# Kernel tuning notes

Hardware: AMD Instinct MI355X
Metric: run time of the kernel (lower is better)

Reference implementation:

```python
import jax, jax.numpy as jnp
import numpy as np
import math

NHEAD = 16
FACTOR = 5


def setup_inputs() -> dict:
    key = jax.random.key(0)
    ks = jax.random.split(key, 10)
    B, L, Dm = 2, 2048, 1024
    x = jax.random.normal(ks[0], (B, L, Dm), dtype=jnp.float32)
    w = lambda k: jax.random.normal(k, (Dm, Dm), dtype=jnp.float32) * 0.02
    b = lambda k: jax.random.normal(k, (Dm,), dtype=jnp.float32) * 0.02
    return {
        "x": x,
        "Wq": w(ks[1]), "bq": b(ks[2]),
        "Wk": w(ks[3]), "bk": b(ks[4]),
        "Wv": w(ks[5]), "bv": b(ks[6]),
        "Wo": w(ks[7]), "bo": b(ks[8]),
    }


def reference(x, Wq, bq, Wk, bk, Wv, bv, Wo, bo):
    B, L, Dm = x.shape
    H = NHEAD
    D = Dm // H
    # U = number of top scores kept per query row (ProbSparse sparsity level)
    U = min(L, int(FACTOR * math.log(L)) if L > 1 else L)

    def proj(W, b):
        # torch Linear: x @ W^T + b ; then [B,L,H,D] -> [B,H,L,D]
        return (x @ W.T + b).reshape(B, L, H, D).transpose(0, 2, 1, 3)

    Q = proj(Wq, bq)
    K = proj(Wk, bk)
    V = proj(Wv, bv)

    scores = jnp.einsum("bhqd,bhkd->bhqk", Q, K) / math.sqrt(D)  # [B,H,L,L]
    # kth-largest score per row; keep entries >= threshold (ties kept, matching torch semantics)
    thresh = jax.lax.top_k(scores, U)[0][..., -1:]  # [B,H,L,1]
    scores = jnp.where(scores < thresh, -jnp.inf, scores)
    attn = jax.nn.softmax(scores, axis=-1)  # dropout is identity in eval
    context = jnp.einsum("bhqk,bhkd->bhqd", attn, V)
    context = context.transpose(0, 2, 1, 3).reshape(B, L, Dm)
    return context @ Wo.T + bo
```

## Files before the change

### kernel.cpp

```cpp
#include <hip/hip_runtime.h>
#include <math.h>

#define BB 2
#define LL 2048
#define DM 1024
#define NH 16
#define HD 64

__device__ __forceinline__ unsigned mono32(float f) {
    unsigned u = __float_as_uint(f);
    return (u & 0x80000000u) ? ~u : (u | 0x80000000u);
}
__device__ __forceinline__ float unmono32(unsigned m) {
    const unsigned u = (m & 0x80000000u) ? (m & 0x7FFFFFFFu) : ~m;
    return __uint_as_float(u);
}

__global__ __launch_bounds__(256) void transpose1024(
    const float* __restrict__ in, float* __restrict__ out)
{
    __shared__ float t[32][33];
    const int bx = blockIdx.x * 32, by = blockIdx.y * 32;
    const int tx = threadIdx.x & 31, ty = threadIdx.x >> 5;
    for (int r = ty; r < 32; r += 8)
        t[r][tx] = in[(size_t)(by + r) * DM + bx + tx];
    __syncthreads();
    for (int r = ty; r < 32; r += 8)
        out[(size_t)(bx + r) * DM + by + tx] = t[tx][r];
}

__global__ __launch_bounds__(256) void proj_emul(
    const float* __restrict__ x, const float* __restrict__ Wt,
    const float* __restrict__ bias, float* __restrict__ outp)
{
    __shared__ float xs[8][DM];
    const int tid = threadIdx.x;
    const int n   = blockIdx.x * 256 + tid;
    const int m0  = blockIdx.y * 8;

    for (int i = tid; i < 8 * 256; i += 256) {
        const int r = i >> 8, c4 = (i & 255) << 2;
        *(float4*)&xs[r][c4] = *(const float4*)&x[(size_t)(m0 + r) * DM + c4];
    }
    __syncthreads();

    const int kbound[4] = {0, 384, 704, 1024};

    float S[8] = {0, 0, 0, 0, 0, 0, 0, 0};
#pragma unroll
    for (int p = 0; p < 3; p++) {
        float P[8] = {0, 0, 0, 0, 0, 0, 0, 0};
        for (int k = kbound[p]; k < kbound[p + 1]; k++) {
            const float w = Wt[(size_t)k * DM + n];
#pragma unroll
            for (int m = 0; m < 8; m++) P[m] = fmaf(xs[m][k], w, P[m]);
        }
#pragma unroll
        for (int m = 0; m < 8; m++) S[m] += P[m];
    }

    const int h = n / HD, d = n % HD;
#pragma unroll
    for (int m = 0; m < 8; m++) {
        const int mm = m0 + m;
        const int b = mm / LL, l = mm % LL;
        outp[(((size_t)b * NH + h) * LL + l) * HD + d] = S[m] + bias[n];
    }
}

template <int MODE>
__global__ __launch_bounds__(256) void gemm_f32(
    const float* __restrict__ A, const float* __restrict__ W,
    const float* __restrict__ bias, float* __restrict__ out,
    int M, int N, int K)
{
    __shared__ float As[16][64];
    __shared__ float Bs[16][64];
    const int tid = threadIdx.x;
    const int m0 = blockIdx.y * 64;
    const int n0 = blockIdx.x * 64;
    const int tx = tid & 15, ty = tid >> 4;
    const int lr = tid >> 2, lc = (tid & 3) * 4;

    float acc[4][4] = {};

    for (int k0 = 0; k0 < K; k0 += 16) {
        float4 a4 = *(const float4*)&A[(size_t)(m0 + lr) * K + k0 + lc];
        float4 b4 = *(const float4*)&W[(size_t)(n0 + lr) * K + k0 + lc];
        __syncthreads();
        As[lc + 0][lr] = a4.x; As[lc + 1][lr] = a4.y;
        As[lc + 2][lr] = a4.z; As[lc + 3][lr] = a4.w;
        Bs[lc + 0][lr] = b4.x; Bs[lc + 1][lr] = b4.y;
        Bs[lc + 2][lr] = b4.z; Bs[lc + 3][lr] = b4.w;
        __syncthreads();
#pragma unroll
        for (int kk = 0; kk < 16; kk++) {
            float4 av = *(const float4*)&As[kk][ty * 4];
            float4 bv = *(const float4*)&Bs[kk][tx * 4];
            float a[4] = {av.x, av.y, av.z, av.w};
            float b[4] = {bv.x, bv.y, bv.z, bv.w};
#pragma unroll
            for (int i = 0; i < 4; i++)
#pragma unroll
                for (int j = 0; j < 4; j++)
                    acc[i][j] = fmaf(a[i], b[j], acc[i][j]);
        }
    }

#pragma unroll
    for (int i = 0; i < 4; i++) {
        const int m = m0 + ty * 4 + i;
#pragma unroll
        for (int j = 0; j < 4; j++) {
            const int n = n0 + tx * 4 + j;
            const float v = acc[i][j] + bias[n];
            if (MODE == 0) {
                const int b = m / LL, l = m % LL;
                const int h = n / HD, d = n % HD;
                out[(((size_t)b * NH + h) * LL + l) * HD + d] = v;
            } else {
                out[(size_t)m * N + n] = v;
            }
        }
    }
}

__global__ __launch_bounds__(256) void score_np(
    const float* __restrict__ Qf, const float* __restrict__ Kf,
    unsigned* __restrict__ scw, int bh0)
{
#pragma clang fp contract(off)
    const int tid  = threadIdx.x;
    const int lane = tid & 63;
    const int wv   = tid >> 6;
    const int l0   = blockIdx.x * 8;
    const int bhl  = blockIdx.y;
    const int bh   = bh0 + bhl;

    __shared__ float kt[2][64][68];
    __shared__ float qsh[8][64];

    const float* __restrict__ Kb = Kf + (size_t)bh * LL * HD;

    if (tid < 128) {
        const int r = tid >> 4, d4 = tid & 15;
        *(float4*)&qsh[r][d4 * 4] =
            *(const float4*)&Qf[((size_t)bh * LL + l0 + r) * HD + d4 * 4];
    }
#pragma unroll
    for (int i = 0; i < 4; i++) {
        const int idx = i * 256 + tid;
        *(float4*)&kt[0][idx >> 4][(idx & 15) * 4] =
            *(const float4*)&Kb[(size_t)(idx >> 4) * HD + (idx & 15) * 4];
    }
    __syncthreads();

    const int r0 = wv * 2, r1 = r0 + 1;
    unsigned* __restrict__ s0 = scw + ((size_t)bhl * LL + l0 + r0) * LL;
    unsigned* __restrict__ s1 = scw + ((size_t)bhl * LL + l0 + r1) * LL;

    for (int tile = 0; tile < 32; tile++) {
        const int buf = tile & 1;
        float4 pf0, pf1, pf2, pf3;
        if (tile < 31) {
            const float* src = Kb + (size_t)(tile + 1) * 64 * HD;
            pf0 = *(const float4*)&src[(size_t)((0 * 256 + tid) >> 4) * HD + ((0 * 256 + tid) & 15) * 4];
            pf1 = *(const float4*)&src[(size_t)((1 * 256 + tid) >> 4) * HD + ((1 * 256 + tid) & 15) * 4];
            pf2 = *(const float4*)&src[(size_t)((2 * 256 + tid) >> 4) * HD + ((2 * 256 + tid) & 15) * 4];
            pf3 = *(const float4*)&src[(size_t)((3 * 256 + tid) >> 4) * HD + ((3 * 256 + tid) & 15) * 4];
        }

        float axA = 0, ayA = 0, azA = 0, awA = 0;
        float axB = 0, ayB = 0, azB = 0, awB = 0;
        const float* krow = &kt[buf][lane][0];
        const float* qA = &qsh[r0][0];
        const float* qB = &qsh[r1][0];
#pragma unroll
        for (int t = 0; t < 4; t++) {
#pragma unroll
            for (int sub = 3; sub >= 0; sub--) {
                const int d4 = 4 * t + sub;
                const float4 kf = *(const float4*)&krow[d4 * 4];
                const float4 qa = *(const float4*)&qA[d4 * 4];
                const float4 qb = *(const float4*)&qB[d4 * 4];
                axA = qa.x * kf.x + axA; ayA = qa.y * kf.y + ayA;
                azA = qa.z * kf.z + azA; awA = qa.w * kf.w + awA;
                axB = qb.x * kf.x + axB; ayB = qb.y * kf.y + ayB;
                azB = qb.z * kf.z + azB; awB = qb.w * kf.w + awB;
            }
        }
        s0[tile * 64 + lane] = mono32(((axA + ayA) + (azA + awA)) * 0.125f);
        s1[tile * 64 + lane] = mono32(((axB + ayB) + (azB + awB)) * 0.125f);

        if (tile < 31) {
            *(float4*)&kt[buf ^ 1][(0 * 256 + tid) >> 4][((0 * 256 + tid) & 15) * 4] = pf0;
            *(float4*)&kt[buf ^ 1][(1 * 256 + tid) >> 4][((1 * 256 + tid) & 15) * 4] = pf1;
            *(float4*)&kt[buf ^ 1][(2 * 256 + tid) >> 4][((2 * 256 + tid) & 15) * 4] = pf2;
            *(float4*)&kt[buf ^ 1][(3 * 256 + tid) >> 4][((3 * 256 + tid) & 15) * 4] = pf3;
            __syncthreads();
        }
    }
}

__global__ __launch_bounds__(256) void select_np(
    const unsigned* __restrict__ scw, const float* __restrict__ Vf,
    float* __restrict__ ctx, int U, int bh0)
{
#pragma clang fp contract(off)
    const int tid  = threadIdx.x;
    const int lane = tid & 63;
    const int wv   = tid >> 6;
    const int l0   = blockIdx.x * 8;
    const int bhl  = blockIdx.y;
    const int bh   = bh0 + bhl;
    const int b    = bh / NH;
    const int h    = bh % NH;

    __shared__ float wls[8][64];
    __shared__ int   kls[8][64];

    const unsigned long long laneLT = (1ull << lane) - 1ull;
    const float* __restrict__ Vb = Vf + (size_t)bh * LL * HD;

#pragma unroll
    for (int rr8 = 0; rr8 < 2; rr8++) {
        const int rr = wv * 2 + rr8;
        const unsigned* __restrict__ srow =
            scw + ((size_t)bhl * LL + l0 + rr) * LL;

        unsigned mv[32];
#pragma unroll
        for (int j = 0; j < 32; j++) mv[j] = srow[lane + 64 * j];

        unsigned lo = 0u, hi = 0xFFFFFFFFu;
        while (lo < hi) {
            const unsigned span = hi - lo;
            const unsigned mid = lo + (span >> 1) + (span & 1u);
            int c = 0;
#pragma unroll
            for (int j = 0; j < 32; j++)
                c += (int)__popcll(__ballot(mv[j] >= mid));
            if (c >= U) lo = mid; else hi = mid - 1u;
        }

        unsigned mk = 0;
#pragma unroll
        for (int j = 0; j < 32; j++)
            if (mv[j] >= lo) mk = (mv[j] > mk) ? mv[j] : mk;
#pragma unroll
        for (int off = 32; off > 0; off >>= 1) {
            const unsigned o = __shfl_xor(mk, off, 64);
            mk = (o > mk) ? o : mk;
        }
        const float mx = unmono32(mk);

        int n = 0;
#pragma unroll
        for (int j = 0; j < 32; j++) {
            const bool p = (mv[j] >= lo);
            const unsigned long long ball = __ballot(p);
            if (p) {
                const int pos = n + (int)__popcll(ball & laneLT);
                if (pos < 64) {
                    kls[rr][pos] = lane + 64 * j;
                    wls[rr][pos] = expf(unmono32(mv[j]) - mx);
                }
            }
            n += (int)__popcll(ball);
        }
        if (n > 64) n = 64;

        float dl = (lane < n) ? wls[rr][lane] : 0.0f;
#pragma unroll
        for (int off = 32; off > 0; off >>= 1) dl += __shfl_xor(dl, off, 64);
        const float rden = 1.0f / dl;

        float acc = 0.0f;
        for (int c = 0; c < n; c++)
            acc = fmaf(wls[rr][c], Vb[(size_t)kls[rr][c] * HD + lane], acc);

        ctx[((size_t)b * LL + l0 + rr) * DM + h * HD + lane] = acc * rden;
    }
}

extern "C" void kernel_launch(void* const* d_in, const int* in_sizes, int n_in,
                              void* d_out, int out_size, void* d_ws, size_t ws_size,
                              hipStream_t stream)
{
    const float* x  = (const float*)d_in[0];
    const float* Wq = (const float*)d_in[1];
    const float* bq = (const float*)d_in[2];
    const float* Wk = (const float*)d_in[3];
    const float* bk = (const float*)d_in[4];
    const float* Wv = (const float*)d_in[5];
    const float* bv = (const float*)d_in[6];
    const float* Wo = (const float*)d_in[7];
    const float* bo = (const float*)d_in[8];
    float* out = (float*)d_out;

    const size_t E = (size_t)BB * NH * LL * HD;
    float* Wt1 = (float*)d_ws;
    float* Wt2 = Wt1 + (size_t)DM * DM;
    float* Qf  = Wt2 + (size_t)DM * DM;
    float* Kf  = Qf + E;
    float* Vf  = Kf + E;
    float* ctx = Vf + E;
    unsigned* scw = (unsigned*)(ctx + E);

    int U = (int)(5.0 * log((double)LL));
    if (U > LL) U = LL;

    const size_t base_bytes = (size_t)72 * 1024 * 1024;
    const size_t per_bh = (size_t)LL * LL * 4;
    size_t avail = (ws_size > base_bytes) ? (ws_size - base_bytes) : 0;
    int chunk = (int)(avail / per_bh);
    if (chunk < 1) chunk = 1;
    if (chunk > 8) chunk = 8;

    const int M = BB * LL;
    dim3 blk(256);
    dim3 gT(DM / 32, DM / 32);
    dim3 gP(DM / 256, M / 8);
    dim3 g64(DM / 64, M / 64);

    hipLaunchKernelGGL(transpose1024, gT, blk, 0, stream, Wq, Wt1);
    hipLaunchKernelGGL(transpose1024, gT, blk, 0, stream, Wk, Wt2);
    hipLaunchKernelGGL(proj_emul, gP, blk, 0, stream, x, Wt1, bq, Qf);
    hipLaunchKernelGGL(proj_emul, gP, blk, 0, stream, x, Wt2, bk, Kf);
    hipLaunchKernelGGL((gemm_f32<0>), g64, blk, 0, stream, x, Wv, bv, Vf, M, DM, DM);

    for (int bh0 = 0; bh0 < BB * NH; bh0 += chunk) {
        int nb = BB * NH - bh0;
        if (nb > chunk) nb = chunk;
        dim3 gA(LL / 8, nb);
        hipLaunchKernelGGL(score_np,  gA, blk, 0, stream, Qf, Kf, scw, bh0);
        hipLaunchKernelGGL(select_np, gA, blk, 0, stream, scw, Vf, ctx, U, bh0);
    }

    hipLaunchKernelGGL((gemm_f32<1>), g64, blk, 0, stream, ctx, Wo, bo, out, M, DM, DM);
}
```

Measured before the change: 1.948 ms.

## Increase per-thread tiling in projection and score kernels for more data reuse

The projection kernel now has each block cover all output columns for 8 rows, with each thread computing 4 columns via float4 weight loads and vectorised shared x reads. This removes redundant x staging and cuts per-FMA load overhead. The score kernel processes 16 query rows per block (4 per wave), so each K tile loaded into shared memory is reused twice as much. The cost is higher register pressure and fewer blocks in both kernels.

```diff
diff --git a/kernel.cpp b/kernel.cpp
--- a/kernel.cpp
+++ b/kernel.cpp
@@ -35,8 +35,8 @@
 {
     __shared__ float xs[8][DM];
     const int tid = threadIdx.x;
-    const int n   = blockIdx.x * 256 + tid;
-    const int m0  = blockIdx.y * 8;
+    const int n4  = tid * 4;
+    const int m0  = blockIdx.x * 8;
 
     for (int i = tid; i < 8 * 256; i += 256) {
         const int r = i >> 8, c4 = (i & 255) << 2;
@@ -45,26 +45,53 @@
     __syncthreads();
 
     const int kbound[4] = {0, 384, 704, 1024};
-
-    float S[8] = {0, 0, 0, 0, 0, 0, 0, 0};
+    float S[8][4] = {};
 #pragma unroll
     for (int p = 0; p < 3; p++) {
-        float P[8] = {0, 0, 0, 0, 0, 0, 0, 0};
-        for (int k = kbound[p]; k < kbound[p + 1]; k++) {
-            const float w = Wt[(size_t)k * DM + n];
-#pragma unroll
-            for (int m = 0; m < 8; m++) P[m] = fmaf(xs[m][k], w, P[m]);
-        }
-#pragma unroll
-        for (int m = 0; m < 8; m++) S[m] += P[m];
-    }
-
-    const int h = n / HD, d = n % HD;
+        float P[8][4] = {};
+        for (int k = kbound[p]; k < kbound[p + 1]; k += 4) {
+            const float4 w0 = *(const float4*)&Wt[(size_t)(k + 0) * DM + n4];
+            const float4 w1 = *(const float4*)&Wt[(size_t)(k + 1) * DM + n4];
+            const float4 w2 = *(const float4*)&Wt[(size_t)(k + 2) * DM + n4];
+            const float4 w3 = *(const float4*)&Wt[(size_t)(k + 3) * DM + n4];
+#pragma unroll
+            for (int m = 0; m < 8; m++) {
+                const float4 xv = *(const float4*)&xs[m][k];
+                P[m][0] = fmaf(xv.x, w0.x, P[m][0]);
+                P[m][1] = fmaf(xv.x, w0.y, P[m][1]);
+                P[m][2] = fmaf(xv.x, w0.z, P[m][2]);
+                P[m][3] = fmaf(xv.x, w0.w, P[m][3]);
+                P[m][0] = fmaf(xv.y, w1.x, P[m][0]);
+                P[m][1] = fmaf(xv.y, w1.y, P[m][1]);
+                P[m][2] = fmaf(xv.y, w1.z, P[m][2]);
+                P[m][3] = fmaf(xv.y, w1.w, P[m][3]);
+                P[m][0] = fmaf(xv.z, w2.x, P[m][0]);
+                P[m][1] = fmaf(xv.z, w2.y, P[m][1]);
+                P[m][2] = fmaf(xv.z, w2.z, P[m][2]);
+                P[m][3] = fmaf(xv.z, w2.w, P[m][3]);
+                P[m][0] = fmaf(xv.w, w3.x, P[m][0]);
+                P[m][1] = fmaf(xv.w, w3.y, P[m][1]);
+                P[m][2] = fmaf(xv.w, w3.z, P[m][2]);
+                P[m][3] = fmaf(xv.w, w3.w, P[m][3]);
+            }
+        }
+#pragma unroll
+        for (int m = 0; m < 8; m++) {
+#pragma unroll
+            for (int j = 0; j < 4; j++) S[m][j] += P[m][j];
+        }
+    }
+
+    const float4 b4v = *(const float4*)&bias[n4];
+    const int h = n4 / HD, d0 = n4 % HD;
 #pragma unroll
     for (int m = 0; m < 8; m++) {
         const int mm = m0 + m;
         const int b = mm / LL, l = mm % LL;
-        outp[(((size_t)b * NH + h) * LL + l) * HD + d] = S[m] + bias[n];
+        float4 o;
+        o.x = S[m][0] + b4v.x; o.y = S[m][1] + b4v.y;
+        o.z = S[m][2] + b4v.z; o.w = S[m][3] + b4v.w;
+        *(float4*)&outp[(((size_t)b * NH + h) * LL + l) * HD + d0] = o;
     }
 }
 
@@ -133,19 +160,19 @@
     const int tid  = threadIdx.x;
     const int lane = tid & 63;
     const int wv   = tid >> 6;
-    const int l0   = blockIdx.x * 8;
+    const int l0   = blockIdx.x * 16;
     const int bhl  = blockIdx.y;
     const int bh   = bh0 + bhl;
 
     __shared__ float kt[2][64][68];
-    __shared__ float qsh[8][64];
+    __shared__ float qsh[16][64];
 
     const float* __restrict__ Kb = Kf + (size_t)bh * LL * HD;
 
-    if (tid < 128) {
-        const int r = tid >> 4, d4 = tid & 15;
-        *(float4*)&qsh[r][d4 * 4] =
-            *(const float4*)&Qf[((size_t)bh * LL + l0 + r) * HD + d4 * 4];
+    {
+        const int r = tid >> 4, d4q = tid & 15;
+        *(float4*)&qsh[r][d4q * 4] =
+            *(const float4*)&Qf[((size_t)bh * LL + l0 + r) * HD + d4q * 4];
     }
 #pragma unroll
     for (int i = 0; i < 4; i++) {
@@ -155,9 +182,11 @@
     }
     __syncthreads();
 
-    const int r0 = wv * 2, r1 = r0 + 1;
-    unsigned* __restrict__ s0 = scw + ((size_t)bhl * LL + l0 + r0) * LL;
-    unsigned* __restrict__ s1 = scw + ((size_t)bhl * LL + l0 + r1) * LL;
+    const int r0 = wv * 4;
+    unsigned* __restrict__ s0 = scw + ((size_t)bhl * LL + l0 + r0 + 0) * LL;
+    unsigned* __restrict__ s1 = scw + ((size_t)bhl * LL + l0 + r0 + 1) * LL;
+    unsigned* __restrict__ s2 = scw + ((size_t)bhl * LL + l0 + r0 + 2) * LL;
+    unsigned* __restrict__ s3 = scw + ((size_t)bhl * LL + l0 + r0 + 3) * LL;
 
     for (int tile = 0; tile < 32; tile++) {
         const int buf = tile & 1;
@@ -170,27 +199,39 @@
             pf3 = *(const float4*)&src[(size_t)((3 * 256 + tid) >> 4) * HD + ((3 * 256 + tid) & 15) * 4];
         }
 
-        float axA = 0, ayA = 0, azA = 0, awA = 0;
-        float axB = 0, ayB = 0, azB = 0, awB = 0;
+        float ax0 = 0, ay0 = 0, az0 = 0, aw0 = 0;
+        float ax1 = 0, ay1 = 0, az1 = 0, aw1 = 0;
+        float ax2 = 0, ay2 = 0, az2 = 0, aw2 = 0;
+        float ax3 = 0, ay3 = 0, az3 = 0, aw3 = 0;
         const float* krow = &kt[buf][lane][0];
-        const float* qA = &qsh[r0][0];
-        const float* qB = &qsh[r1][0];
+        const float* q0 = &qsh[r0 + 0][0];
+        const float* q1 = &qsh[r0 + 1][0];
+        const float* q2 = &qsh[r0 + 2][0];
+        const float* q3 = &qsh[r0 + 3][0];
 #pragma unroll
         for (int t = 0; t < 4; t++) {
 #pragma unroll
             for (int sub = 3; sub >= 0; sub--) {
                 const int d4 = 4 * t + sub;
                 const float4 kf = *(const float4*)&krow[d4 * 4];
-                const float4 qa = *(const float4*)&qA[d4 * 4];
-                const float4 qb = *(const float4*)&qB[d4 * 4];
-                axA = qa.x * kf.x + axA; ayA = qa.y * kf.y + ayA;
-                azA = qa.z * kf.z + azA; awA = qa.w * kf.w + awA;
-                axB = qb.x * kf.x + axB; ayB = qb.y * kf.y + ayB;
-                azB = qb.z * kf.z + azB; awB = qb.w * kf.w + awB;
+                const float4 qa = *(const float4*)&q0[d4 * 4];
+                const float4 qb = *(const float4*)&q1[d4 * 4];
+                const float4 qc = *(const float4*)&q2[d4 * 4];
+                const float4 qd = *(const float4*)&q3[d4 * 4];
+                ax0 = qa.x * kf.x + ax0; ay0 = qa.y * kf.y + ay0;
+                az0 = qa.z * kf.z + az0; aw0 = qa.w * kf.w + aw0;
+                ax1 = qb.x * kf.x + ax1; ay1 = qb.y * kf.y + ay1;
+                az1 = qb.z * kf.z + az1; aw1 = qb.w * kf.w + aw1;
+                ax2 = qc.x * kf.x + ax2; ay2 = qc.y * kf.y + ay2;
+                az2 = qc.z * kf.z + az2; aw2 = qc.w * kf.w + aw2;
+                ax3 = qd.x * kf.x + ax3; ay3 = qd.y * kf.y + ay3;
+                az3 = qd.z * kf.z + az3; aw3 = qd.w * kf.w + aw3;
             }
         }
-        s0[tile * 64 + lane] = mono32(((axA + ayA) + (azA + awA)) * 0.125f);
-        s1[tile * 64 + lane] = mono32(((axB + ayB) + (azB + awB)) * 0.125f);
+        s0[tile * 64 + lane] = mono32(((ax0 + ay0) + (az0 + aw0)) * 0.125f);
+        s1[tile * 64 + lane] = mono32(((ax1 + ay1) + (az1 + aw1)) * 0.125f);
+        s2[tile * 64 + lane] = mono32(((ax2 + ay2) + (az2 + aw2)) * 0.125f);
+        s3[tile * 64 + lane] = mono32(((ax3 + ay3) + (az3 + aw3)) * 0.125f);
 
         if (tile < 31) {
             *(float4*)&kt[buf ^ 1][(0 * 256 + tid) >> 4][((0 * 256 + tid) & 15) * 4] = pf0;
@@ -320,7 +361,7 @@
     const int M = BB * LL;
     dim3 blk(256);
     dim3 gT(DM / 32, DM / 32);
-    dim3 gP(DM / 256, M / 8);
+    dim3 gP(M / 8);
     dim3 g64(DM / 64, M / 64);
 
     hipLaunchKernelGGL(transpose1024, gT, blk, 0, stream, Wq, Wt1);
@@ -332,9 +373,10 @@
     for (int bh0 = 0; bh0 < BB * NH; bh0 += chunk) {
         int nb = BB * NH - bh0;
         if (nb > chunk) nb = chunk;
-        dim3 gA(LL / 8, nb);
+        dim3 gA(LL / 16, nb);
+        dim3 gS(LL / 8, nb);
         hipLaunchKernelGGL(score_np,  gA, blk, 0, stream, Qf, Kf, scw, bh0);
-        hipLaunchKernelGGL(select_np, gA, blk, 0, stream, scw, Vf, ctx, U, bh0);
+        hipLaunchKernelGGL(select_np, gS, blk, 0, stream, scw, Vf, ctx, U, bh0);
     }
 
     hipLaunchKernelGGL((gemm_f32<1>), g64, blk, 0, stream, ctx, Wo, bo, out, M, DM, DM);
```

Measured after the change: 1.681 ms. 1.16x faster.
